# Kernel tuning notes

Hardware: AMD Instinct MI355X
Metric: run time of the kernel (lower is better)

The kernel has to match this reference:

```python
import jax, jax.numpy as jnp
import numpy as np

N_NODES = 50000
N_EDGES = 1600000
N_GRAPHS = 64
IN_DIM = 128
HID = 128
N_CLASSES = 10


def setup_inputs() -> dict:
    key = jax.random.key(0)
    ks = jax.random.split(key, 12)
    x = jax.random.normal(ks[0], (N_NODES, IN_DIM), dtype=jnp.float32)
    edge_index = jax.random.randint(ks[1], (2, N_EDGES), 0, N_NODES, dtype=jnp.int32)
    batch = jnp.sort(jax.random.randint(ks[2], (N_NODES,), 0, N_GRAPHS, dtype=jnp.int32))
    def glorot(k, shape):
        s = 1.0 / np.sqrt(shape[0])
        return jax.random.uniform(k, shape, jnp.float32, -s, s)
    W1 = glorot(ks[3], (IN_DIM, HID)); b1 = jnp.zeros((HID,), jnp.float32)
    W2 = glorot(ks[4], (HID, HID));    b2 = jnp.zeros((HID,), jnp.float32)
    Wc1 = glorot(ks[5], (HID, HID));   bc1 = glorot(ks[6], (HID,))
    Wc2 = glorot(ks[7], (HID, N_CLASSES)); bc2 = glorot(ks[8], (N_CLASSES,))
    return {"x": x, "edge_index": edge_index, "batch": batch,
            "W1": W1, "b1": b1, "W2": W2, "b2": b2,
            "Wc1": Wc1, "bc1": bc1, "Wc2": Wc2, "bc2": bc2}


def gcn_conv(x, edge_index, W, b):
    """PyG GCNConv: sym-normalized A-hat (with self loops) @ (x W) + b."""
    n = x.shape[0]
    loop = jnp.arange(n, dtype=edge_index.dtype)
    src = jnp.concatenate([edge_index[0], loop])  # message source
    dst = jnp.concatenate([edge_index[1], loop])  # message target
    deg = jax.ops.segment_sum(jnp.ones_like(src, dtype=x.dtype), dst, num_segments=n)
    dinv = jnp.where(deg > 0, jax.lax.rsqrt(deg), jnp.zeros_like(deg))
    norm = dinv[src] * dinv[dst]  # [E+N]
    h = x @ W                     # [N, H]
    msg = h[src] * norm[:, None]  # gather + scale
    out = jax.ops.segment_sum(msg, dst, num_segments=n)
    return out + b


def reference(x, edge_index, batch, W1, b1, W2, b2, Wc1, bc1, Wc2, bc2):
    h = jax.nn.relu(gcn_conv(x, edge_index, W1, b1))
    h = jax.nn.relu(gcn_conv(h, edge_index, W2, b2))
    # per-graph mean pooling (segment mean)
    sums = jax.ops.segment_sum(h, batch, num_segments=N_GRAPHS)
    cnt = jax.ops.segment_sum(jnp.ones((h.shape[0],), h.dtype), batch, num_segments=N_GRAPHS)
    g = sums / jnp.clip(cnt, 1.0)[:, None]  # [G, H]
    z = jax.nn.relu(g @ Wc1 + bc1)
    return z @ Wc2 + bc2
```

## Files before the change

kernel.cpp:

```cpp
#include <hip/hip_runtime.h>
#include <cstdint>
#include <cstddef>

#define CHUNK 8192

typedef __attribute__((ext_vector_type(8))) short short8;
typedef __attribute__((ext_vector_type(4))) float f32x4;
typedef __attribute__((ext_vector_type(2))) float f32x2;
typedef __attribute__((ext_vector_type(4))) unsigned int u32x4;

__device__ __forceinline__ float bf2f(unsigned short u) {
  return __uint_as_float(((unsigned)u) << 16);
}
__device__ __forceinline__ unsigned short f2bf(float f) {
  unsigned u = __float_as_uint(f);
  u += 0x7fffu + ((u >> 16) & 1u);
  return (unsigned short)(u >> 16);
}
__device__ __forceinline__ f32x2 unpk(unsigned u) {
  f32x2 r;
  r.x = __uint_as_float(u << 16);
  r.y = __uint_as_float(u & 0xffff0000u);
  return r;
}
__device__ __forceinline__ void pkfma(f32x2& a, f32x2 b, f32x2 c) {
  asm("v_pk_fma_f32 %0, %1, %2, %0" : "+v"(a) : "v"(b), "v"(c));
}

union SMemX {
  unsigned short ws[128 * 136];
  struct { unsigned sorted[CHUNK];
           int h[256]; int lps[256]; int base_s[256]; int cur[256]; } sc;
  struct { int c[256]; int cur[256]; int sb[256];
           unsigned short colL[12288]; } cf;
};

__global__ void prep_k(const float* __restrict__ W1, const float* __restrict__ W2,
                       unsigned short* __restrict__ W1t, unsigned short* __restrict__ W2t,
                       int* __restrict__ gcur, int B,
                       float* __restrict__ gsums, int GN) {
  int idx = blockIdx.x * 256 + threadIdx.x;
  const float* W = (idx < 16384) ? W1 : W2;
  unsigned short* Wt = (idx < 16384) ? W1t : W2t;
  int i = idx & 16383;
  int k = i >> 7, n = i & 127;
  Wt[n * 128 + k] = f2bf(W[i]);
  if (blockIdx.x == 0 && threadIdx.x < B) gcur[threadIdx.x] = 0;
  if (idx < GN) gsums[idx] = 0.f;
}

template <bool AF32, bool WF32>
__device__ __forceinline__ void gemm_tile(SMemX& sm, const void* Ap,
                                          const void* Wp,
                                          unsigned short* C, int N, int tile) {
  if (WF32) {
    const float* Wf = (const float*)Wp;
    for (int idx = threadIdx.x; idx < 16384; idx += 512) {
      int k = idx >> 7, n = idx & 127;
      sm.ws[n * 136 + k] = f2bf(Wf[idx]);
    }
  } else {
    const unsigned short* Wt = (const unsigned short*)Wp;
    for (int idx = threadIdx.x; idx < 2048; idx += 512) {
      int n = idx >> 4, c = idx & 15;
      *(uint4*)&sm.ws[n * 136 + c * 8] = ((const uint4*)Wt)[idx];
    }
  }
  __syncthreads();
  const int w = threadIdx.x >> 6;
  const int lane = threadIdx.x & 63;
  const int quad = lane >> 4, l16 = lane & 15;
  const int r = tile * 128 + w * 16 + l16;
  f32x4 acc[8] = {};
  #pragma unroll
  for (int ks = 0; ks < 4; ks++) {
    short8 a = {};
    if (r < N) {
      if (AF32) {
        const float* ar = (const float*)Ap + (size_t)r * 128 + ks * 32 + quad * 8;
        float4 u0 = *(const float4*)ar;
        float4 u1 = *(const float4*)(ar + 4);
        a[0] = (short)f2bf(u0.x); a[1] = (short)f2bf(u0.y);
        a[2] = (short)f2bf(u0.z); a[3] = (short)f2bf(u0.w);
        a[4] = (short)f2bf(u1.x); a[5] = (short)f2bf(u1.y);
        a[6] = (short)f2bf(u1.z); a[7] = (short)f2bf(u1.w);
      } else {
        a = *(const short8*)((const unsigned short*)Ap + (size_t)r * 128 + ks * 32 + quad * 8);
      }
    }
    #pragma unroll
    for (int t = 0; t < 8; t++) {
      short8 bF = *(const short8*)&sm.ws[(t * 16 + l16) * 136 + ks * 32 + quad * 8];
      acc[t] = __builtin_amdgcn_mfma_f32_16x16x32_bf16(a, bF, acc[t], 0, 0, 0);
    }
  }
  __syncthreads();
  unsigned short* Cs = sm.ws;
  {
    int rloc = w * 16 + quad * 4;
    #pragma unroll
    for (int t = 0; t < 8; t++)
      #pragma unroll
      for (int rg = 0; rg < 4; rg++)
        Cs[(rloc + rg) * 132 + t * 16 + l16] = f2bf(acc[t][rg]);
  }
  __syncthreads();
  const int r0 = tile * 128;
  for (int idx = threadIdx.x; idx < 2048; idx += 512) {
    int row = idx >> 4, c = idx & 15;
    int rr = r0 + row;
    if (rr < N) {
      uint2 a = *(uint2*)&Cs[row * 132 + c * 8];
      uint2 b = *(uint2*)&Cs[row * 132 + c * 8 + 4];
      ((uint4*)C)[(size_t)rr * 16 + c] = make_uint4(a.x, a.y, b.x, b.y);
    }
  }
}

__global__ __launch_bounds__(512) void scat_gemm1a_k(const int* __restrict__ src,
                                                     const int* __restrict__ dst, int E,
                                                     int* __restrict__ gcur,
                                                     unsigned int* __restrict__ tmp,
                                                     int cap, int B,
                                                     const float* __restrict__ x,
                                                     const float* __restrict__ W1,
                                                     unsigned short* __restrict__ B2, int N,
                                                     int nblk, int T1,
                                                     const float* __restrict__ W2,
                                                     unsigned short* __restrict__ W2t,
                                                     int P2) {
  __shared__ SMemX sm;
  const int t = threadIdx.x;
  const int bid = blockIdx.x;
  if (bid >= nblk) {
    int gb = bid - nblk;
    if (gb < T1) {
      gemm_tile<true, true>(sm, x, W1, B2, N, gb);
    } else {
      int base = (gb - T1) * 512 + t;
      for (int i = base; i < 16384; i += P2 * 512) {
        int k = i >> 7, n = i & 127;
        W2t[n * 128 + k] = f2bf(W2[i]);
      }
    }
    return;
  }
  if (t < 256) sm.sc.h[t] = 0;
  __syncthreads();
  int e0 = bid * CHUNK;
  int e1 = e0 + CHUNK; if (e1 > E) e1 = E;
  int m = e1 - e0;
  for (int i = t; i < m; i += 512) {
    atomicAdd(&sm.sc.h[dst[e0 + i] >> 8], 1);
  }
  __syncthreads();
  int v = (t < 256) ? sm.sc.h[t] : 0;
  if (t < 256) sm.sc.lps[t] = v;
  __syncthreads();
  for (int off = 1; off < 256; off <<= 1) {
    int u = (t >= off && t < 256) ? sm.sc.lps[t - off] : 0;
    __syncthreads();
    if (t < 256) sm.sc.lps[t] += u;
    __syncthreads();
  }
  int incl = (t < 256) ? sm.sc.lps[t] : 0;
  if (t < B && v > 0) sm.sc.base_s[t] = atomicAdd(&gcur[t], v);
  if (t < 256) {
    sm.sc.cur[t] = 0;
    sm.sc.lps[t] = incl - v;
  }
  __syncthreads();
  for (int i = t; i < m; i += 512) {
    int d = dst[e0 + i], s = src[e0 + i];
    int b = d >> 8;
    int r = atomicAdd(&sm.sc.cur[b], 1);
    sm.sc.sorted[sm.sc.lps[b] + r] = ((unsigned)b << 24) | ((unsigned)s << 8) | (unsigned)(d & 255);
  }
  __syncthreads();
  for (int i = t; i < m; i += 512) {
    unsigned u = sm.sc.sorted[i];
    int b = u >> 24;
    int p = sm.sc.base_s[b] + (i - sm.sc.lps[b]);
    if (p < cap) tmp[(size_t)b * cap + p] = u;
  }
}

__global__ __launch_bounds__(512) void cnt_gemm1b_k(const unsigned int* __restrict__ tmp,
                                                    const int* __restrict__ gcur,
                                                    int N, int E, int cap, int B,
                                                    float* __restrict__ dinv,
                                                    int* __restrict__ rs,
                                                    unsigned short* __restrict__ col,
                                                    const float* __restrict__ x,
                                                    const float* __restrict__ W1,
                                                    unsigned short* __restrict__ B2,
                                                    int T1) {
  __shared__ SMemX sm;
  const int t = threadIdx.x;
  if ((int)blockIdx.x >= B) {
    gemm_tile<true, true>(sm, x, W1, B2, N, T1 + (int)blockIdx.x - B);
    return;
  }
  int b = blockIdx.x;
  int cb = 0;
  if (t < B) { cb = gcur[t]; if (cb > cap) cb = cap; }
  if (t < 256) sm.cf.sb[t] = cb;
  __syncthreads();
  for (int off = 1; off < 256; off <<= 1) {
    int u = (t >= off && t < 256) ? sm.cf.sb[t - off] : 0;
    __syncthreads();
    if (t < 256) sm.cf.sb[t] += u;
    __syncthreads();
  }
  int base_b = (b > 0) ? sm.cf.sb[b - 1] : 0;
  int cnt_b = sm.cf.sb[b] - base_b;
  if (b == 0 && t == 0) rs[N] = sm.cf.sb[B - 1];
  const unsigned* tb = tmp + (size_t)b * cap;
  if (t < 256) sm.cf.c[t] = 0;
  __syncthreads();
  for (int i = t; i < cnt_b; i += 512) atomicAdd(&sm.cf.c[tb[i] & 255u], 1);
  __syncthreads();
  int v = (t < 256) ? sm.cf.c[t] : 0;
  if (t < 256) sm.cf.cur[t] = v;
  __syncthreads();
  for (int off = 1; off < 256; off <<= 1) {
    int u = (t >= off && t < 256) ? sm.cf.cur[t - off] : 0;
    __syncthreads();
    if (t < 256) sm.cf.cur[t] += u;
    __syncthreads();
  }
  int rsv = (t < 256) ? (base_b + sm.cf.cur[t] - v) : 0;
  int node = (b << 8) + t;
  if (t < 256 && node < N) {
    rs[node] = rsv;
    dinv[node] = rsqrtf((float)v + 1.0f);
  }
  __syncthreads();
  if (cnt_b <= 12288) {
    if (t < 256) sm.cf.cur[t] = rsv - base_b;
    __syncthreads();
    for (int i = t; i < cnt_b; i += 512) {
      unsigned u = tb[i];
      int lpos = atomicAdd(&sm.cf.cur[u & 255u], 1);
      sm.cf.colL[lpos] = (unsigned short)((u >> 8) & 0xFFFFu);
    }
    __syncthreads();
    for (int i = t; i < cnt_b; i += 512) col[base_b + i] = sm.cf.colL[i];
  } else {
    if (t < 256) sm.cf.cur[t] = rsv;
    __syncthreads();
    for (int i = t; i < cnt_b; i += 512) {
      unsigned u = tb[i];
      int pos = atomicAdd(&sm.cf.cur[u & 255u], 1);
      col[pos] = (unsigned short)((u >> 8) & 0xFFFFu);
    }
  }
}

template <bool AF32, bool WF32>
__global__ __launch_bounds__(512) void gemm_bf_k(const void* __restrict__ Ap,
                                                 const void* __restrict__ Wp,
                                                 unsigned short* __restrict__ C, int N) {
  __shared__ SMemX sm;
  gemm_tile<AF32, WF32>(sm, Ap, Wp, C, N, blockIdx.x);
}

template <typename CT>
__device__ __forceinline__ void agg_body(f32x2 (&acc2)[4],
                                         const unsigned short* __restrict__ h,
                                         const CT* __restrict__ col,
                                         const float* __restrict__ dinv,
                                         int beg, int end, int g, int l) {
  int base = beg;
  for (; base + 32 <= end; base += 32) {
    int s[8];
    float w[8];
    uint4 H[8];
    #pragma unroll
    for (int k = 0; k < 8; k++) s[k] = (int)col[base + 4 * k + g];
    #pragma unroll
    for (int k = 0; k < 8; k++) w[k] = dinv[s[k]];
    #pragma unroll
    for (int k = 0; k < 8; k++) H[k] = ((const uint4*)(h + (size_t)s[k] * 128))[l];
    #pragma unroll
    for (int k = 0; k < 8; k++) {
      f32x2 wv; wv.x = w[k]; wv.y = w[k];
      pkfma(acc2[0], unpk(H[k].x), wv);
      pkfma(acc2[1], unpk(H[k].y), wv);
      pkfma(acc2[2], unpk(H[k].z), wv);
      pkfma(acc2[3], unpk(H[k].w), wv);
    }
  }
  for (; base < end; base += 16) {
    int e0 = base + g, e1 = base + 4 + g, e2 = base + 8 + g, e3 = base + 12 + g;
    int i0 = (e0 < end) ? e0 : end - 1;
    int i1 = (e1 < end) ? e1 : end - 1;
    int i2 = (e2 < end) ? e2 : end - 1;
    int i3 = (e3 < end) ? e3 : end - 1;
    int s0 = (int)col[i0], s1 = (int)col[i1], s2 = (int)col[i2], s3 = (int)col[i3];
    float w0 = (e0 < end) ? dinv[s0] : 0.f;
    float w1 = (e1 < end) ? dinv[s1] : 0.f;
    float w2 = (e2 < end) ? dinv[s2] : 0.f;
    float w3 = (e3 < end) ? dinv[s3] : 0.f;
    uint4 h0 = ((const uint4*)(h + (size_t)s0 * 128))[l];
    uint4 h1 = ((const uint4*)(h + (size_t)s1 * 128))[l];
    uint4 h2 = ((const uint4*)(h + (size_t)s2 * 128))[l];
    uint4 h3 = ((const uint4*)(h + (size_t)s3 * 128))[l];
    f32x2 w0v; w0v.x = w0; w0v.y = w0;
    f32x2 w1v; w1v.x = w1; w1v.y = w1;
    f32x2 w2v; w2v.x = w2; w2v.y = w2;
    f32x2 w3v; w3v.x = w3; w3v.y = w3;
    pkfma(acc2[0], unpk(h0.x), w0v); pkfma(acc2[0], unpk(h1.x), w1v);
    pkfma(acc2[0], unpk(h2.x), w2v); pkfma(acc2[0], unpk(h3.x), w3v);
    pkfma(acc2[1], unpk(h0.y), w0v); pkfma(acc2[1], unpk(h1.y), w1v);
    pkfma(acc2[1], unpk(h2.y), w2v); pkfma(acc2[1], unpk(h3.y), w3v);
    pkfma(acc2[2], unpk(h0.z), w0v); pkfma(acc2[2], unpk(h1.z), w1v);
    pkfma(acc2[2], unpk(h2.z), w2v); pkfma(acc2[2], unpk(h3.z), w3v);
    pkfma(acc2[3], unpk(h0.w), w0v); pkfma(acc2[3], unpk(h1.w), w1v);
    pkfma(acc2[3], unpk(h2.w), w2v); pkfma(acc2[3], unpk(h3.w), w3v);
  }
  #pragma unroll
  for (int j = 0; j < 4; j++) {
    acc2[j].x += __shfl_xor(acc2[j].x, 16);
    acc2[j].y += __shfl_xor(acc2[j].y, 16);
    acc2[j].x += __shfl_xor(acc2[j].x, 32);
    acc2[j].y += __shfl_xor(acc2[j].y, 32);
  }
}

template <typename CT>
__global__ __launch_bounds__(256) void agg32_k(const unsigned short* __restrict__ h,
                                               const int* __restrict__ rs,
                                               const CT* __restrict__ col,
                                               const float* __restrict__ dinv,
                                               const float* __restrict__ bias,
                                               unsigned short* __restrict__ outp, int n) {
  int wid = (blockIdx.x * blockDim.x + threadIdx.x) >> 6;
  int lane = threadIdx.x & 63;
  if (wid >= n) return;
  const int g = lane >> 4;
  const int l = lane & 15;
  float di = dinv[wid];
  f32x2 acc2[4];
  {
    uint4 sv = ((const uint4*)(h + (size_t)wid * 128))[l];
    float ws = (g == 0) ? di : 0.f;
    f32x2 wv; wv.x = ws; wv.y = ws;
    acc2[0] = unpk(sv.x) * wv;
    acc2[1] = unpk(sv.y) * wv;
    acc2[2] = unpk(sv.z) * wv;
    acc2[3] = unpk(sv.w) * wv;
  }
  agg_body<CT>(acc2, h, col, dinv, rs[wid], rs[wid + 1], g, l);
  if (g == 0) {
    float4 bA = *(const float4*)(bias + l * 8);
    float4 bB = *(const float4*)(bias + l * 8 + 4);
    float r0 = fmaxf(acc2[0].x * di + bA.x, 0.f);
    float r1 = fmaxf(acc2[0].y * di + bA.y, 0.f);
    float r2 = fmaxf(acc2[1].x * di + bA.z, 0.f);
    float r3 = fmaxf(acc2[1].y * di + bA.w, 0.f);
    float r4 = fmaxf(acc2[2].x * di + bB.x, 0.f);
    float r5 = fmaxf(acc2[2].y * di + bB.y, 0.f);
    float r6 = fmaxf(acc2[3].x * di + bB.z, 0.f);
    float r7 = fmaxf(acc2[3].y * di + bB.w, 0.f);
    u32x4 v;
    v.x = (unsigned)f2bf(r0) | ((unsigned)f2bf(r1) << 16);
    v.y = (unsigned)f2bf(r2) | ((unsigned)f2bf(r3) << 16);
    v.z = (unsigned)f2bf(r4) | ((unsigned)f2bf(r5) << 16);
    v.w = (unsigned)f2bf(r6) | ((unsigned)f2bf(r7) << 16);
    __builtin_nontemporal_store(v, (u32x4*)outp + (size_t)wid * 16 + l);
  }
}

#define SPLITS 8
__global__ __launch_bounds__(256) void pool_sum_k(const unsigned short* __restrict__ h,
                                                  const int* __restrict__ bat, int n,
                                                  float* __restrict__ gsums) {
  __shared__ float red[16][136];
  const int g = blockIdx.x / SPLITS;
  const int sp = blockIdx.x % SPLITS;
  const int t = threadIdx.x;
  const int slot = t >> 4;
  const int seg = t & 15;
  int lo;
  {
    int l = 0, r = n;
    while (l < r) { int m = (l + r) >> 1; if (bat[m] < g) l = m + 1; else r = m; }
    lo = l;
  }
  int hi;
  {
    int l = lo, r = n;
    while (l < r) { int m = (l + r) >> 1; if (bat[m] < g + 1) l = m + 1; else r = m; }
    hi = l;
  }
  int L = hi - lo;
  int chunk = (L + SPLITS - 1) / SPLITS;
  int i0 = lo + sp * chunk;
  int i1 = i0 + chunk; if (i1 > hi) i1 = hi;
  if (i0 >= i1) return;
  float a0 = 0.f, a1 = 0.f, a2 = 0.f, a3 = 0.f, a4 = 0.f, a5 = 0.f, a6 = 0.f, a7 = 0.f;
  for (int i = i0 + slot; i < i1; i += 16) {
    uint4 v = ((const uint4*)(h + (size_t)i * 128))[seg];
    a0 += bf2f((unsigned short)v.x);  a1 += bf2f((unsigned short)(v.x >> 16));
    a2 += bf2f((unsigned short)v.y);  a3 += bf2f((unsigned short)(v.y >> 16));
    a4 += bf2f((unsigned short)v.z);  a5 += bf2f((unsigned short)(v.z >> 16));
    a6 += bf2f((unsigned short)v.w);  a7 += bf2f((unsigned short)(v.w >> 16));
  }
  red[slot][seg * 8 + 0] = a0; red[slot][seg * 8 + 1] = a1;
  red[slot][seg * 8 + 2] = a2; red[slot][seg * 8 + 3] = a3;
  red[slot][seg * 8 + 4] = a4; red[slot][seg * 8 + 5] = a5;
  red[slot][seg * 8 + 6] = a6; red[slot][seg * 8 + 7] = a7;
  __syncthreads();
  if (t < 128) {
    float s = 0.f;
    #pragma unroll
    for (int k = 0; k < 16; k++) s += red[k][t];
    unsafeAtomicAdd(&gsums[g * 128 + t], s);
  }
}

__global__ __launch_bounds__(256) void classify_k(const float* __restrict__ gsums,
                                                  const int* __restrict__ bat, int n,
                                                  const float* __restrict__ Wc1,
                                                  const float* __restrict__ bc1,
                                                  const float* __restrict__ Wc2,
                                                  const float* __restrict__ bc2,
                                                  float* __restrict__ out, int nc) {
  __shared__ float gs[128];
  __shared__ float zs[128];
  const int g = blockIdx.x;
  const int t = threadIdx.x;
  int lo;
  {
    int l = 0, r = n;
    while (l < r) { int m = (l + r) >> 1; if (bat[m] < g) l = m + 1; else r = m; }
    lo = l;
  }
  int hi;
  {
    int l = lo, r = n;
    while (l < r) { int m = (l + r) >> 1; if (bat[m] < g + 1) l = m + 1; else r = m; }
    hi = l;
  }
  if (t < 128) {
    float c = (float)(hi - lo); if (c < 1.f) c = 1.f;
    gs[t] = gsums[g * 128 + t] / c;
  }
  __syncthreads();
  if (t < 128) {
    float a = bc1[t];
    for (int k = 0; k < 128; k++) a += gs[k] * Wc1[k * 128 + t];
    zs[t] = fmaxf(a, 0.f);
  }
  __syncthreads();
  if (t < nc) {
    float o = bc2[t];
    for (int k = 0; k < 128; k++) o += zs[k] * Wc2[k * nc + t];
    out[g * nc + t] = o;
  }
}

__global__ __launch_bounds__(256) void poolclassify2_k(const unsigned short* __restrict__ h,
                                                       const int* __restrict__ bat, int n,
                                                       const float* __restrict__ Wc1,
                                                       const float* __restrict__ bc1,
                                                       const float* __restrict__ Wc2,
                                                       const float* __restrict__ bc2,
                                                       float* __restrict__ out, int nc) {
  __shared__ float red[16][136];
  __shared__ float gs[128];
  __shared__ float zs[128];
  const int g = blockIdx.x;
  const int t = threadIdx.x;
  const int slot = t >> 4;
  const int seg = t & 15;
  int lo;
  {
    int l = 0, r = n;
    while (l < r) { int m = (l + r) >> 1; if (bat[m] < g) l = m + 1; else r = m; }
    lo = l;
  }
  int hi;
  {
    int l = lo, r = n;
    while (l < r) { int m = (l + r) >> 1; if (bat[m] < g + 1) l = m + 1; else r = m; }
    hi = l;
  }
  float a0 = 0.f, a1 = 0.f, a2 = 0.f, a3 = 0.f, a4 = 0.f, a5 = 0.f, a6 = 0.f, a7 = 0.f;
  for (int i = lo + slot; i < hi; i += 16) {
    uint4 v = ((const uint4*)(h + (size_t)i * 128))[seg];
    a0 += bf2f((unsigned short)v.x);  a1 += bf2f((unsigned short)(v.x >> 16));
    a2 += bf2f((unsigned short)v.y);  a3 += bf2f((unsigned short)(v.y >> 16));
    a4 += bf2f((unsigned short)v.z);  a5 += bf2f((unsigned short)(v.z >> 16));
    a6 += bf2f((unsigned short)v.w);  a7 += bf2f((unsigned short)(v.w >> 16));
  }
  red[slot][seg * 8 + 0] = a0; red[slot][seg * 8 + 1] = a1;
  red[slot][seg * 8 + 2] = a2; red[slot][seg * 8 + 3] = a3;
  red[slot][seg * 8 + 4] = a4; red[slot][seg * 8 + 5] = a5;
  red[slot][seg * 8 + 6] = a6; red[slot][seg * 8 + 7] = a7;
  __syncthreads();
  if (t < 128) {
    float c = (float)(hi - lo); if (c < 1.f) c = 1.f;
    float s = 0.f;
    #pragma unroll
    for (int k = 0; k < 16; k++) s += red[k][t];
    gs[t] = s / c;
  }
  __syncthreads();
  if (t < 128) {
    float a = bc1[t];
    for (int k = 0; k < 128; k++) a += gs[k] * Wc1[k * 128 + t];
    zs[t] = fmaxf(a, 0.f);
  }
  __syncthreads();
  if (t < nc) {
    float o = bc2[t];
    for (int k = 0; k < 128; k++) o += zs[k] * Wc2[k * nc + t];
    out[g * nc + t] = o;
  }
}

__global__ void count_edges_k(const int* __restrict__ dst, int E, int* __restrict__ cnt) {
  int e = blockIdx.x * blockDim.x + threadIdx.x;
  if (e < E) atomicAdd(&cnt[dst[e]], 1);
}
__global__ void dinv_k(const int* __restrict__ cnt, float* __restrict__ dinv, int n) {
  int i = blockIdx.x * blockDim.x + threadIdx.x;
  if (i < n) dinv[i] = rsqrtf((float)cnt[i] + 1.0f);
}
__global__ void fill_csr_k(const int* __restrict__ src, const int* __restrict__ dst, int E,
                           int* __restrict__ cursor, int* __restrict__ col) {
  int e = blockIdx.x * blockDim.x + threadIdx.x;
  if (e < E) {
    int d = dst[e], s = src[e];
    int pos = atomicAdd(&cursor[d], 1);
    col[pos] = s;
  }
}
__global__ void scan1_k(const int* __restrict__ cnt, int* __restrict__ rs,
                        int* __restrict__ partials, int n) {
  __shared__ int s[1024];
  int t = threadIdx.x;
  int gid = blockIdx.x * 1024 + t;
  int v = (gid < n) ? cnt[gid] : 0;
  s[t] = v;
  __syncthreads();
  for (int off = 1; off < 1024; off <<= 1) {
    int u = (t >= off) ? s[t - off] : 0;
    __syncthreads();
    s[t] += u;
    __syncthreads();
  }
  if (gid < n) rs[gid] = s[t] - v;
  if (t == 1023) partials[blockIdx.x] = s[1023];
}
__global__ void scan2_k(int* __restrict__ partials, int nb) {
  if (threadIdx.x == 0 && blockIdx.x == 0) {
    int acc = 0;
    for (int i = 0; i < nb; i++) { int v = partials[i]; partials[i] = acc; acc += v; }
  }
}
__global__ void scan3_k(int* __restrict__ rs, int* __restrict__ cursor,
                        const int* __restrict__ partials, int n, int total) {
  int gid = blockIdx.x * blockDim.x + threadIdx.x;
  if (gid < n) {
    int v = rs[gid] + partials[gid >> 10];
    rs[gid] = v;
    cursor[gid] = v;
  }
  if (gid == 0) rs[n] = total;
}

extern "C" void kernel_launch(void* const* d_in, const int* in_sizes, int n_in,
                              void* d_out, int out_size, void* d_ws, size_t ws_size,
                              hipStream_t stream) {
  const float* x   = (const float*)d_in[0];
  const int*   ei  = (const int*)d_in[1];
  const int*   bat = (const int*)d_in[2];
  const float* W1  = (const float*)d_in[3];
  const float* b1  = (const float*)d_in[4];
  const float* W2  = (const float*)d_in[5];
  const float* b2  = (const float*)d_in[6];
  const float* Wc1 = (const float*)d_in[7];
  const float* bc1 = (const float*)d_in[8];
  const float* Wc2 = (const float*)d_in[9];
  const float* bc2 = (const float*)d_in[10];
  float* out = (float*)d_out;

  const int N  = in_sizes[0] / 128;
  const int E  = in_sizes[1] / 2;
  const int NC = in_sizes[10];
  const int G  = out_size / NC;
  const int* src = ei;
  const int* dst = ei + E;
  (void)n_in; (void)ws_size;

  size_t off = 0;
  auto walloc = [&](size_t bytes) -> void* {
    void* p = (char*)d_ws + off;
    off += (bytes + 255) & ~(size_t)255;
    return p;
  };
  unsigned short* B2 = (unsigned short*)walloc((size_t)N * 128 * 2);
  unsigned short* B3 = (unsigned short*)walloc((size_t)N * 128 * 2);
  unsigned short* W1t = (unsigned short*)walloc(128 * 128 * 2);
  unsigned short* W2t = (unsigned short*)walloc(128 * 128 * 2);
  float* dinv = (float*)walloc((size_t)N * 4);
  int*   rs   = (int*)  walloc((size_t)(N + 1) * 4);
  float* gsums = (float*)walloc((size_t)G * 128 * 4);
  int*   gcur  = (int*)walloc(256 * 4);

  const bool small = (N <= 65535);
  const int gblocks = (N + 127) / 128;
  const int aggGrid = (N + 3) / 4;

  if (small) {
    const int B    = (N + 255) >> 8;
    const int nblk = (E + CHUNK - 1) / CHUNK;
    const int cap  = (E + B - 1) / B + 2048;
    const int T1   = (gblocks * 3) / 5;
    const int P2   = 8;
    unsigned short* col = (unsigned short*)walloc((size_t)E * 2);
    unsigned int*   tmp = (unsigned int*)  walloc((size_t)B * cap * 4);

    (void)hipMemsetAsync(gsums, 0, (size_t)G * 128 * 4 + 1024, stream);
    scat_gemm1a_k<<<nblk + T1 + P2, 512, 0, stream>>>(src, dst, E, gcur, tmp, cap, B,
                                                      x, W1, B2, N, nblk, T1, W2, W2t, P2);
    cnt_gemm1b_k<<<B + (gblocks - T1), 512, 0, stream>>>(tmp, gcur, N, E, cap, B,
                                                         dinv, rs, col, x, W1, B2, T1);
    agg32_k<unsigned short><<<aggGrid, 256, 0, stream>>>(B2, rs, col, dinv, b1, B3, N);
    gemm_bf_k<false, false><<<gblocks, 512, 0, stream>>>(B3, W2t, B2, N);
    agg32_k<unsigned short><<<aggGrid, 256, 0, stream>>>(B2, rs, col, dinv, b2, B3, N);
    pool_sum_k<<<G * SPLITS, 256, 0, stream>>>(B3, bat, N, gsums);
    classify_k<<<G, 256, 0, stream>>>(gsums, bat, N, Wc1, bc1, Wc2, bc2, out, NC);
  } else {
    const int nb = (N + 1023) / 1024;
    int* cnt    = (int*)walloc((size_t)N * 4);
    int* cursor = (int*)walloc((size_t)N * 4);
    int* col    = (int*)walloc((size_t)E * 4);
    int* partials = (int*)walloc(256 * 4);
    prep_k<<<128, 256, 0, stream>>>(W1, W2, W1t, W2t, cnt , 0, gsums, G * 128);
    (void)hipMemsetAsync(cnt, 0, (size_t)N * 4, stream);
    count_edges_k<<<(E + 255) / 256, 256, 0, stream>>>(dst, E, cnt);
    scan1_k<<<nb, 1024, 0, stream>>>(cnt, rs, partials, N);
    scan2_k<<<1, 64, 0, stream>>>(partials, nb);
    scan3_k<<<(N + 255) / 256, 256, 0, stream>>>(rs, cursor, partials, N, E);
    dinv_k<<<(N + 255) / 256, 256, 0, stream>>>(cnt, dinv, N);
    fill_csr_k<<<(E + 255) / 256, 256, 0, stream>>>(src, dst, E, cursor, col);

    gemm_bf_k<true, false><<<gblocks, 512, 0, stream>>>(x, W1t, B2, N);
    agg32_k<int><<<aggGrid, 256, 0, stream>>>(B2, rs, col, dinv, b1, B3, N);
    gemm_bf_k<false, false><<<gblocks, 512, 0, stream>>>(B3, W2t, B2, N);
    agg32_k<int><<<aggGrid, 256, 0, stream>>>(B2, rs, col, dinv, b2, B3, N);
    poolclassify2_k<<<G, 256, 0, stream>>>(B3, bat, N, Wc1, bc1, Wc2, bc2, out, NC);
  }
}
```

Before: 259.2 us.

## Fuse full GCN pipeline into one cooperative persistent kernel with grid syncs

```diff
diff --git a/kernel.cpp b/kernel.cpp
--- a/kernel.cpp
+++ b/kernel.cpp
@@ -1,8 +1,12 @@
 #include <hip/hip_runtime.h>
+#include <hip/hip_cooperative_groups.h>
 #include <cstdint>
 #include <cstddef>
 
+namespace cg = cooperative_groups;
+
 #define CHUNK 8192
+#define SPLITS 8
 
 typedef __attribute__((ext_vector_type(8))) short short8;
 typedef __attribute__((ext_vector_type(4))) float f32x4;
@@ -33,21 +37,9 @@
            int h[256]; int lps[256]; int base_s[256]; int cur[256]; } sc;
   struct { int c[256]; int cur[256]; int sb[256];
            unsigned short colL[12288]; } cf;
+  struct { float red[16][136]; } pl;
+  struct { float gs[128]; float zs[128]; } cl;
 };
-
-__global__ void prep_k(const float* __restrict__ W1, const float* __restrict__ W2,
-                       unsigned short* __restrict__ W1t, unsigned short* __restrict__ W2t,
-                       int* __restrict__ gcur, int B,
-                       float* __restrict__ gsums, int GN) {
-  int idx = blockIdx.x * 256 + threadIdx.x;
-  const float* W = (idx < 16384) ? W1 : W2;
-  unsigned short* Wt = (idx < 16384) ? W1t : W2t;
-  int i = idx & 16383;
-  int k = i >> 7, n = i & 127;
-  Wt[n * 128 + k] = f2bf(W[i]);
-  if (blockIdx.x == 0 && threadIdx.x < B) gcur[threadIdx.x] = 0;
-  if (idx < GN) gsums[idx] = 0.f;
-}
 
 template <bool AF32, bool WF32>
 __device__ __forceinline__ void gemm_tile(SMemX& sm, const void* Ap,
@@ -117,37 +109,15 @@
   }
 }
 
-__global__ __launch_bounds__(512) void scat_gemm1a_k(const int* __restrict__ src,
-                                                     const int* __restrict__ dst, int E,
-                                                     int* __restrict__ gcur,
-                                                     unsigned int* __restrict__ tmp,
-                                                     int cap, int B,
-                                                     const float* __restrict__ x,
-                                                     const float* __restrict__ W1,
-                                                     unsigned short* __restrict__ B2, int N,
-                                                     int nblk, int T1,
-                                                     const float* __restrict__ W2,
-                                                     unsigned short* __restrict__ W2t,
-                                                     int P2) {
-  __shared__ SMemX sm;
+__device__ __forceinline__ void scatter_block(SMemX& sm, const int* __restrict__ src,
+                                              const int* __restrict__ dst, int E,
+                                              int* __restrict__ gcur,
+                                              unsigned int* __restrict__ tmp,
+                                              int cap, int B, int cblk) {
   const int t = threadIdx.x;
-  const int bid = blockIdx.x;
-  if (bid >= nblk) {
-    int gb = bid - nblk;
-    if (gb < T1) {
-      gemm_tile<true, true>(sm, x, W1, B2, N, gb);
-    } else {
-      int base = (gb - T1) * 512 + t;
-      for (int i = base; i < 16384; i += P2 * 512) {
-        int k = i >> 7, n = i & 127;
-        W2t[n * 128 + k] = f2bf(W2[i]);
-      }
-    }
-    return;
-  }
   if (t < 256) sm.sc.h[t] = 0;
   __syncthreads();
-  int e0 = bid * CHUNK;
+  int e0 = cblk * CHUNK;
   int e1 = e0 + CHUNK; if (e1 > E) e1 = E;
   int m = e1 - e0;
   for (int i = t; i < m; i += 512) {
@@ -183,25 +153,16 @@
     int p = sm.sc.base_s[b] + (i - sm.sc.lps[b]);
     if (p < cap) tmp[(size_t)b * cap + p] = u;
   }
-}
-
-__global__ __launch_bounds__(512) void cnt_gemm1b_k(const unsigned int* __restrict__ tmp,
-                                                    const int* __restrict__ gcur,
-                                                    int N, int E, int cap, int B,
-                                                    float* __restrict__ dinv,
-                                                    int* __restrict__ rs,
-                                                    unsigned short* __restrict__ col,
-                                                    const float* __restrict__ x,
-                                                    const float* __restrict__ W1,
-                                                    unsigned short* __restrict__ B2,
-                                                    int T1) {
-  __shared__ SMemX sm;
+  __syncthreads();
+}
+
+__device__ __forceinline__ void cntfill_block(SMemX& sm, const unsigned int* __restrict__ tmp,
+                                              const int* __restrict__ gcur,
+                                              int N, int cap, int B,
+                                              float* __restrict__ dinv,
+                                              int* __restrict__ rs,
+                                              unsigned short* __restrict__ col, int b) {
   const int t = threadIdx.x;
-  if ((int)blockIdx.x >= B) {
-    gemm_tile<true, true>(sm, x, W1, B2, N, T1 + (int)blockIdx.x - B);
-    return;
-  }
-  int b = blockIdx.x;
   int cb = 0;
   if (t < B) { cb = gcur[t]; if (cb > cap) cb = cap; }
   if (t < 256) sm.cf.sb[t] = cb;
@@ -255,14 +216,7 @@
       col[pos] = (unsigned short)((u >> 8) & 0xFFFFu);
     }
   }
-}
-
-template <bool AF32, bool WF32>
-__global__ __launch_bounds__(512) void gemm_bf_k(const void* __restrict__ Ap,
-                                                 const void* __restrict__ Wp,
-                                                 unsigned short* __restrict__ C, int N) {
-  __shared__ SMemX sm;
-  gemm_tile<AF32, WF32>(sm, Ap, Wp, C, N, blockIdx.x);
+  __syncthreads();
 }
 
 template <typename CT>
@@ -329,6 +283,245 @@
 }
 
 template <typename CT>
+__device__ __forceinline__ void agg_phase(const unsigned short* __restrict__ h,
+                                          const int* __restrict__ rs,
+                                          const CT* __restrict__ col,
+                                          const float* __restrict__ dinv,
+                                          const float* __restrict__ bias,
+                                          unsigned short* __restrict__ outp,
+                                          int n, int bid, int NB) {
+  const int t = threadIdx.x;
+  const int w = t >> 6;
+  const int lane = t & 63;
+  const int g = lane >> 4;
+  const int l = lane & 15;
+  for (int wid = bid * 8 + w; wid < n; wid += NB * 8) {
+    float di = dinv[wid];
+    f32x2 acc2[4];
+    {
+      uint4 sv = ((const uint4*)(h + (size_t)wid * 128))[l];
+      float ws = (g == 0) ? di : 0.f;
+      f32x2 wv; wv.x = ws; wv.y = ws;
+      acc2[0] = unpk(sv.x) * wv;
+      acc2[1] = unpk(sv.y) * wv;
+      acc2[2] = unpk(sv.z) * wv;
+      acc2[3] = unpk(sv.w) * wv;
+    }
+    agg_body<CT>(acc2, h, col, dinv, rs[wid], rs[wid + 1], g, l);
+    if (g == 0) {
+      float4 bA = *(const float4*)(bias + l * 8);
+      float4 bB = *(const float4*)(bias + l * 8 + 4);
+      float r0 = fmaxf(acc2[0].x * di + bA.x, 0.f);
+      float r1 = fmaxf(acc2[0].y * di + bA.y, 0.f);
+      float r2 = fmaxf(acc2[1].x * di + bA.z, 0.f);
+      float r3 = fmaxf(acc2[1].y * di + bA.w, 0.f);
+      float r4 = fmaxf(acc2[2].x * di + bB.x, 0.f);
+      float r5 = fmaxf(acc2[2].y * di + bB.y, 0.f);
+      float r6 = fmaxf(acc2[3].x * di + bB.z, 0.f);
+      float r7 = fmaxf(acc2[3].y * di + bB.w, 0.f);
+      u32x4 v;
+      v.x = (unsigned)f2bf(r0) | ((unsigned)f2bf(r1) << 16);
+      v.y = (unsigned)f2bf(r2) | ((unsigned)f2bf(r3) << 16);
+      v.z = (unsigned)f2bf(r4) | ((unsigned)f2bf(r5) << 16);
+      v.w = (unsigned)f2bf(r6) | ((unsigned)f2bf(r7) << 16);
+      __builtin_nontemporal_store(v, (u32x4*)outp + (size_t)wid * 16 + l);
+    }
+  }
+}
+
+__device__ __forceinline__ void pool_block(SMemX& sm, const unsigned short* __restrict__ h,
+                                           const int* __restrict__ bat, int n,
+                                           float* __restrict__ gsums, int s) {
+  const int t = threadIdx.x;
+  const int g = s / SPLITS;
+  const int sp = s % SPLITS;
+  const int slot = (t >> 4) & 15;
+  const int seg = t & 15;
+  int lo;
+  { int l = 0, r = n; while (l < r) { int m = (l + r) >> 1; if (bat[m] < g) l = m + 1; else r = m; } lo = l; }
+  int hi;
+  { int l = lo, r = n; while (l < r) { int m = (l + r) >> 1; if (bat[m] < g + 1) l = m + 1; else r = m; } hi = l; }
+  int L = hi - lo;
+  int chunk = (L + SPLITS - 1) / SPLITS;
+  int i0 = lo + sp * chunk;
+  int i1 = i0 + chunk; if (i1 > hi) i1 = hi;
+  if (i0 >= i1) return;
+  if (t < 256) {
+    float a0 = 0.f, a1 = 0.f, a2 = 0.f, a3 = 0.f, a4 = 0.f, a5 = 0.f, a6 = 0.f, a7 = 0.f;
+    for (int i = i0 + slot; i < i1; i += 16) {
+      uint4 v = ((const uint4*)(h + (size_t)i * 128))[seg];
+      a0 += bf2f((unsigned short)v.x);  a1 += bf2f((unsigned short)(v.x >> 16));
+      a2 += bf2f((unsigned short)v.y);  a3 += bf2f((unsigned short)(v.y >> 16));
+      a4 += bf2f((unsigned short)v.z);  a5 += bf2f((unsigned short)(v.z >> 16));
+      a6 += bf2f((unsigned short)v.w);  a7 += bf2f((unsigned short)(v.w >> 16));
+    }
+    sm.pl.red[slot][seg * 8 + 0] = a0; sm.pl.red[slot][seg * 8 + 1] = a1;
+    sm.pl.red[slot][seg * 8 + 2] = a2; sm.pl.red[slot][seg * 8 + 3] = a3;
+    sm.pl.red[slot][seg * 8 + 4] = a4; sm.pl.red[slot][seg * 8 + 5] = a5;
+    sm.pl.red[slot][seg * 8 + 6] = a6; sm.pl.red[slot][seg * 8 + 7] = a7;
+  }
+  __syncthreads();
+  if (t < 128) {
+    float ssum = 0.f;
+    #pragma unroll
+    for (int k = 0; k < 16; k++) ssum += sm.pl.red[k][t];
+    unsafeAtomicAdd(&gsums[g * 128 + t], ssum);
+  }
+  __syncthreads();
+}
+
+__device__ __forceinline__ void classify_block(SMemX& sm, const float* __restrict__ gsums,
+                                               const int* __restrict__ bat, int n,
+                                               const float* __restrict__ Wc1,
+                                               const float* __restrict__ bc1,
+                                               const float* __restrict__ Wc2,
+                                               const float* __restrict__ bc2,
+                                               float* __restrict__ out, int nc, int g) {
+  const int t = threadIdx.x;
+  int lo;
+  { int l = 0, r = n; while (l < r) { int m = (l + r) >> 1; if (bat[m] < g) l = m + 1; else r = m; } lo = l; }
+  int hi;
+  { int l = lo, r = n; while (l < r) { int m = (l + r) >> 1; if (bat[m] < g + 1) l = m + 1; else r = m; } hi = l; }
+  if (t < 128) {
+    float c = (float)(hi - lo); if (c < 1.f) c = 1.f;
+    sm.cl.gs[t] = gsums[g * 128 + t] / c;
+  }
+  __syncthreads();
+  if (t < 128) {
+    float a = bc1[t];
+    for (int k = 0; k < 128; k++) a += sm.cl.gs[k] * Wc1[k * 128 + t];
+    sm.cl.zs[t] = fmaxf(a, 0.f);
+  }
+  __syncthreads();
+  if (t < nc) {
+    float o = bc2[t];
+    for (int k = 0; k < 128; k++) o += sm.cl.zs[k] * Wc2[k * nc + t];
+    out[g * nc + t] = o;
+  }
+  __syncthreads();
+}
+
+__global__ __launch_bounds__(512) void mega_k(
+    const int* __restrict__ src, const int* __restrict__ dst, int E,
+    int* __restrict__ gcur, unsigned int* __restrict__ tmp, int cap, int B,
+    const float* __restrict__ x, const float* __restrict__ W1,
+    const float* __restrict__ W2,
+    const float* __restrict__ b1v, const float* __restrict__ b2v,
+    const int* __restrict__ bat,
+    const float* __restrict__ Wc1, const float* __restrict__ bc1,
+    const float* __restrict__ Wc2, const float* __restrict__ bc2,
+    float* __restrict__ out, int NC, int G,
+    unsigned short* __restrict__ B2, unsigned short* __restrict__ B3,
+    float* __restrict__ dinv, int* __restrict__ rs,
+    unsigned short* __restrict__ col,
+    float* __restrict__ gsums, int N, int nblk, int gblocks) {
+  __shared__ SMemX sm;
+  cg::grid_group grid = cg::this_grid();
+  const int t = threadIdx.x;
+  const int bid = blockIdx.x;
+  const int NB = gridDim.x;
+  for (int i = bid * 512 + t; i < G * 128; i += NB * 512) gsums[i] = 0.f;
+  if (bid == 0 && t < 256) gcur[t] = 0;
+  grid.sync();
+  for (int c = bid; c < nblk; c += NB) scatter_block(sm, src, dst, E, gcur, tmp, cap, B, c);
+  grid.sync();
+  if (bid < B) {
+    cntfill_block(sm, tmp, gcur, N, cap, B, dinv, rs, col, bid);
+  } else {
+    for (int tile = bid - B; tile < gblocks; tile += NB - B) {
+      gemm_tile<true, true>(sm, x, W1, B2, N, tile);
+      __syncthreads();
+    }
+  }
+  grid.sync();
+  agg_phase<unsigned short>(B2, rs, col, dinv, b1v, B3, N, bid, NB);
+  grid.sync();
+  for (int tile = bid; tile < gblocks; tile += NB) {
+    gemm_tile<false, true>(sm, B3, W2, B2, N, tile);
+    __syncthreads();
+  }
+  grid.sync();
+  agg_phase<unsigned short>(B2, rs, col, dinv, b2v, B3, N, bid, NB);
+  grid.sync();
+  for (int s = bid; s < G * SPLITS; s += NB) pool_block(sm, B3, bat, N, gsums, s);
+  grid.sync();
+  for (int g = bid; g < G; g += NB)
+    classify_block(sm, gsums, bat, N, Wc1, bc1, Wc2, bc2, out, NC, g);
+}
+
+
+__global__ void prep_k(const float* __restrict__ W1, const float* __restrict__ W2,
+                       unsigned short* __restrict__ W1t, unsigned short* __restrict__ W2t,
+                       int* __restrict__ gcur, int B,
+                       float* __restrict__ gsums, int GN) {
+  int idx = blockIdx.x * 256 + threadIdx.x;
+  const float* W = (idx < 16384) ? W1 : W2;
+  unsigned short* Wt = (idx < 16384) ? W1t : W2t;
+  int i = idx & 16383;
+  int k = i >> 7, n = i & 127;
+  Wt[n * 128 + k] = f2bf(W[i]);
+  if (blockIdx.x == 0 && threadIdx.x < B) gcur[threadIdx.x] = 0;
+  if (idx < GN) gsums[idx] = 0.f;
+}
+
+__global__ __launch_bounds__(512) void scat_gemm1a_k(const int* __restrict__ src,
+                                                     const int* __restrict__ dst, int E,
+                                                     int* __restrict__ gcur,
+                                                     unsigned int* __restrict__ tmp,
+                                                     int cap, int B,
+                                                     const float* __restrict__ x,
+                                                     const float* __restrict__ W1,
+                                                     unsigned short* __restrict__ B2, int N,
+                                                     int nblk, int T1,
+                                                     const float* __restrict__ W2,
+                                                     unsigned short* __restrict__ W2t,
+                                                     int P2) {
+  __shared__ SMemX sm;
+  const int t = threadIdx.x;
+  const int bid = blockIdx.x;
+  if (bid >= nblk) {
+    int gb = bid - nblk;
+    if (gb < T1) {
+      gemm_tile<true, true>(sm, x, W1, B2, N, gb);
+    } else {
+      int base = (gb - T1) * 512 + t;
+      for (int i = base; i < 16384; i += P2 * 512) {
+        int k = i >> 7, n = i & 127;
+        W2t[n * 128 + k] = f2bf(W2[i]);
+      }
+    }
+    return;
+  }
+  scatter_block(sm, src, dst, E, gcur, tmp, cap, B, bid);
+}
+
+__global__ __launch_bounds__(512) void cnt_gemm1b_k(const unsigned int* __restrict__ tmp,
+                                                    const int* __restrict__ gcur,
+                                                    int N, int E, int cap, int B,
+                                                    float* __restrict__ dinv,
+                                                    int* __restrict__ rs,
+                                                    unsigned short* __restrict__ col,
+                                                    const float* __restrict__ x,
+                                                    const float* __restrict__ W1,
+                                                    unsigned short* __restrict__ B2,
+                                                    int T1) {
+  __shared__ SMemX sm;
+  if ((int)blockIdx.x >= B) {
+    gemm_tile<true, true>(sm, x, W1, B2, N, T1 + (int)blockIdx.x - B);
+    return;
+  }
+  cntfill_block(sm, tmp, gcur, N, cap, B, dinv, rs, col, blockIdx.x);
+}
+
+template <bool AF32, bool WF32>
+__global__ __launch_bounds__(512) void gemm_bf_k(const void* __restrict__ Ap,
+                                                 const void* __restrict__ Wp,
+                                                 unsigned short* __restrict__ C, int N) {
+  __shared__ SMemX sm;
+  gemm_tile<AF32, WF32>(sm, Ap, Wp, C, N, blockIdx.x);
+}
+
+template <typename CT>
 __global__ __launch_bounds__(256) void agg32_k(const unsigned short* __restrict__ h,
                                                const int* __restrict__ rs,
                                                const CT* __restrict__ col,
@@ -372,7 +565,6 @@
   }
 }
 
-#define SPLITS 8
 __global__ __launch_bounds__(256) void pool_sum_k(const unsigned short* __restrict__ h,
                                                   const int* __restrict__ bat, int n,
                                                   float* __restrict__ gsums) {
@@ -383,17 +575,9 @@
   const int slot = t >> 4;
   const int seg = t & 15;
   int lo;
-  {
-    int l = 0, r = n;
-    while (l < r) { int m = (l + r) >> 1; if (bat[m] < g) l = m + 1; else r = m; }
-    lo = l;
-  }
+  { int l = 0, r = n; while (l < r) { int m = (l + r) >> 1; if (bat[m] < g) l = m + 1; else r = m; } lo = l; }
   int hi;
-  {
-    int l = lo, r = n;
-    while (l < r) { int m = (l + r) >> 1; if (bat[m] < g + 1) l = m + 1; else r = m; }
-    hi = l;
-  }
+  { int l = lo, r = n; while (l < r) { int m = (l + r) >> 1; if (bat[m] < g + 1) l = m + 1; else r = m; } hi = l; }
   int L = hi - lo;
   int chunk = (L + SPLITS - 1) / SPLITS;
   int i0 = lo + sp * chunk;
@@ -432,17 +616,9 @@
   const int g = blockIdx.x;
   const int t = threadIdx.x;
   int lo;
-  {
-    int l = 0, r = n;
-    while (l < r) { int m = (l + r) >> 1; if (bat[m] < g) l = m + 1; else r = m; }
-    lo = l;
-  }
+  { int l = 0, r = n; while (l < r) { int m = (l + r) >> 1; if (bat[m] < g) l = m + 1; else r = m; } lo = l; }
   int hi;
-  {
-    int l = lo, r = n;
-    while (l < r) { int m = (l + r) >> 1; if (bat[m] < g + 1) l = m + 1; else r = m; }
-    hi = l;
-  }
+  { int l = lo, r = n; while (l < r) { int m = (l + r) >> 1; if (bat[m] < g + 1) l = m + 1; else r = m; } hi = l; }
   if (t < 128) {
     float c = (float)(hi - lo); if (c < 1.f) c = 1.f;
     gs[t] = gsums[g * 128 + t] / c;
@@ -476,17 +652,9 @@
   const int slot = t >> 4;
   const int seg = t & 15;
   int lo;
-  {
-    int l = 0, r = n;
-    while (l < r) { int m = (l + r) >> 1; if (bat[m] < g) l = m + 1; else r = m; }
-    lo = l;
-  }
+  { int l = 0, r = n; while (l < r) { int m = (l + r) >> 1; if (bat[m] < g) l = m + 1; else r = m; } lo = l; }
   int hi;
-  {
-    int l = lo, r = n;
-    while (l < r) { int m = (l + r) >> 1; if (bat[m] < g + 1) l = m + 1; else r = m; }
-    hi = l;
-  }
+  { int l = lo, r = n; while (l < r) { int m = (l + r) >> 1; if (bat[m] < g + 1) l = m + 1; else r = m; } hi = l; }
   float a0 = 0.f, a1 = 0.f, a2 = 0.f, a3 = 0.f, a4 = 0.f, a5 = 0.f, a6 = 0.f, a7 = 0.f;
   for (int i = lo + slot; i < hi; i += 16) {
     uint4 v = ((const uint4*)(h + (size_t)i * 128))[seg];
@@ -570,6 +738,50 @@
     cursor[gid] = v;
   }
   if (gid == 0) rs[n] = total;
+}
+
+template <typename CT>
+__global__ __launch_bounds__(256) void agg32i_k(const unsigned short* __restrict__ h,
+                                                const int* __restrict__ rs,
+                                                const CT* __restrict__ col,
+                                                const float* __restrict__ dinv,
+                                                const float* __restrict__ bias,
+                                                unsigned short* __restrict__ outp, int n) {
+  int wid = (blockIdx.x * blockDim.x + threadIdx.x) >> 6;
+  int lane = threadIdx.x & 63;
+  if (wid >= n) return;
+  const int g = lane >> 4;
+  const int l = lane & 15;
+  float di = dinv[wid];
+  f32x2 acc2[4];
+  {
+    uint4 sv = ((const uint4*)(h + (size_t)wid * 128))[l];
+    float ws = (g == 0) ? di : 0.f;
+    f32x2 wv; wv.x = ws; wv.y = ws;
+    acc2[0] = unpk(sv.x) * wv;
+    acc2[1] = unpk(sv.y) * wv;
+    acc2[2] = unpk(sv.z) * wv;
+    acc2[3] = unpk(sv.w) * wv;
+  }
+  agg_body<CT>(acc2, h, col, dinv, rs[wid], rs[wid + 1], g, l);
+  if (g == 0) {
+    float4 bA = *(const float4*)(bias + l * 8);
+    float4 bB = *(const float4*)(bias + l * 8 + 4);
+    float r0 = fmaxf(acc2[0].x * di + bA.x, 0.f);
+    float r1 = fmaxf(acc2[0].y * di + bA.y, 0.f);
+    float r2 = fmaxf(acc2[1].x * di + bA.z, 0.f);
+    float r3 = fmaxf(acc2[1].y * di + bA.w, 0.f);
+    float r4 = fmaxf(acc2[2].x * di + bB.x, 0.f);
+    float r5 = fmaxf(acc2[2].y * di + bB.y, 0.f);
+    float r6 = fmaxf(acc2[3].x * di + bB.z, 0.f);
+    float r7 = fmaxf(acc2[3].y * di + bB.w, 0.f);
+    u32x4 v;
+    v.x = (unsigned)f2bf(r0) | ((unsigned)f2bf(r1) << 16);
+    v.y = (unsigned)f2bf(r2) | ((unsigned)f2bf(r3) << 16);
+    v.z = (unsigned)f2bf(r4) | ((unsigned)f2bf(r5) << 16);
+    v.w = (unsigned)f2bf(r6) | ((unsigned)f2bf(r7) << 16);
+    __builtin_nontemporal_store(v, (u32x4*)outp + (size_t)wid * 16 + l);
+  }
 }
 
 extern "C" void kernel_launch(void* const* d_in, const int* in_sizes, int n_in,
@@ -619,26 +831,70 @@
     const int B    = (N + 255) >> 8;
     const int nblk = (E + CHUNK - 1) / CHUNK;
     const int cap  = (E + B - 1) / B + 2048;
-    const int T1   = (gblocks * 3) / 5;
-    const int P2   = 8;
     unsigned short* col = (unsigned short*)walloc((size_t)E * 2);
     unsigned int*   tmp = (unsigned int*)  walloc((size_t)B * cap * 4);
 
-    (void)hipMemsetAsync(gsums, 0, (size_t)G * 128 * 4 + 1024, stream);
-    scat_gemm1a_k<<<nblk + T1 + P2, 512, 0, stream>>>(src, dst, E, gcur, tmp, cap, B,
-                                                      x, W1, B2, N, nblk, T1, W2, W2t, P2);
-    cnt_gemm1b_k<<<B + (gblocks - T1), 512, 0, stream>>>(tmp, gcur, N, E, cap, B,
-                                                         dinv, rs, col, x, W1, B2, T1);
-    agg32_k<unsigned short><<<aggGrid, 256, 0, stream>>>(B2, rs, col, dinv, b1, B3, N);
-    gemm_bf_k<false, false><<<gblocks, 512, 0, stream>>>(B3, W2t, B2, N);
-    agg32_k<unsigned short><<<aggGrid, 256, 0, stream>>>(B2, rs, col, dinv, b2, B3, N);
-    pool_sum_k<<<G * SPLITS, 256, 0, stream>>>(B3, bat, N, gsums);
-    classify_k<<<G, 256, 0, stream>>>(gsums, bat, N, Wc1, bc1, Wc2, bc2, out, NC);
+    static int s_coopBlocks = -2;
+    if (s_coopBlocks == -2) {
+      s_coopBlocks = -1;
+      int dev = 0;
+      if (hipGetDevice(&dev) == hipSuccess) {
+        hipDeviceProp_t prop;
+        if (hipGetDeviceProperties(&prop, dev) == hipSuccess) {
+          int perCU = 0;
+          if (hipOccupancyMaxActiveBlocksPerMultiprocessor(&perCU, (const void*)mega_k, 512, 0) == hipSuccess && perCU > 0)
+            s_coopBlocks = perCU * prop.multiProcessorCount;
+        }
+      }
+    }
+
+    bool usedCoop = false;
+    if (s_coopBlocks > B + 8) {
+      const int* a_src = src; const int* a_dst = dst; int a_E = E;
+      int* a_gcur = gcur; unsigned int* a_tmp = tmp; int a_cap = cap; int a_B = B;
+      const float* a_x = x; const float* a_W1 = W1; const float* a_W2 = W2;
+      const float* a_b1 = b1; const float* a_b2 = b2; const int* a_bat = bat;
+      const float* a_Wc1 = Wc1; const float* a_bc1 = bc1;
+      const float* a_Wc2 = Wc2; const float* a_bc2 = bc2;
+      float* a_out = out; int a_NC = NC; int a_G = G;
+      unsigned short* a_B2 = B2; unsigned short* a_B3 = B3;
+      float* a_dinv = dinv; int* a_rs = rs; unsigned short* a_col = col;
+      float* a_gsums = gsums; int a_N = N; int a_nblk = nblk; int a_gblocks = gblocks;
+      void* kargs[] = {
+        (void*)&a_src, (void*)&a_dst, (void*)&a_E,
+        (void*)&a_gcur, (void*)&a_tmp, (void*)&a_cap, (void*)&a_B,
+        (void*)&a_x, (void*)&a_W1, (void*)&a_W2,
+        (void*)&a_b1, (void*)&a_b2, (void*)&a_bat,
+        (void*)&a_Wc1, (void*)&a_bc1, (void*)&a_Wc2, (void*)&a_bc2,
+        (void*)&a_out, (void*)&a_NC, (void*)&a_G,
+        (void*)&a_B2, (void*)&a_B3,
+        (void*)&a_dinv, (void*)&a_rs, (void*)&a_col,
+        (void*)&a_gsums, (void*)&a_N, (void*)&a_nblk, (void*)&a_gblocks };
+      if (hipLaunchCooperativeKernel((const void*)mega_k, dim3(s_coopBlocks), dim3(512),
+                                     kargs, 0, stream) == hipSuccess) {
+        usedCoop = true;
+      }
+    }
+
+    if (!usedCoop) {
+      const int T1 = (gblocks * 3) / 5;
+      const int P2 = 8;
+      (void)hipMemsetAsync(gsums, 0, (size_t)G * 128 * 4 + 1024, stream);
+      scat_gemm1a_k<<<nblk + T1 + P2, 512, 0, stream>>>(src, dst, E, gcur, tmp, cap, B,
+                                                        x, W1, B2, N, nblk, T1, W2, W2t, P2);
+      cnt_gemm1b_k<<<B + (gblocks - T1), 512, 0, stream>>>(tmp, gcur, N, E, cap, B,
+                                                           dinv, rs, col, x, W1, B2, T1);
+      agg32_k<unsigned short><<<aggGrid, 256, 0, stream>>>(B2, rs, col, dinv, b1, B3, N);
+      gemm_bf_k<false, false><<<gblocks, 512, 0, stream>>>(B3, W2t, B2, N);
+      agg32_k<unsigned short><<<aggGrid, 256, 0, stream>>>(B2, rs, col, dinv, b2, B3, N);
+      pool_sum_k<<<G * SPLITS, 256, 0, stream>>>(B3, bat, N, gsums);
+      classify_k<<<G, 256, 0, stream>>>(gsums, bat, N, Wc1, bc1, Wc2, bc2, out, NC);
+    }
   } else {
     const int nb = (N + 1023) / 1024;
     int* cnt    = (int*)walloc((size_t)N * 4);
     int* cursor = (int*)walloc((size_t)N * 4);
-    int* col    = (int*)walloc((size_t)E * 4);
+    int* coli   = (int*)walloc((size_t)E * 4);
     int* partials = (int*)walloc(256 * 4);
     prep_k<<<128, 256, 0, stream>>>(W1, W2, W1t, W2t, cnt , 0, gsums, G * 128);
     (void)hipMemsetAsync(cnt, 0, (size_t)N * 4, stream);
@@ -647,12 +903,12 @@
     scan2_k<<<1, 64, 0, stream>>>(partials, nb);
     scan3_k<<<(N + 255) / 256, 256, 0, stream>>>(rs, cursor, partials, N, E);
     dinv_k<<<(N + 255) / 256, 256, 0, stream>>>(cnt, dinv, N);
-    fill_csr_k<<<(E + 255) / 256, 256, 0, stream>>>(src, dst, E, cursor, col);
+    fill_csr_k<<<(E + 255) / 256, 256, 0, stream>>>(src, dst, E, cursor, coli);
 
     gemm_bf_k<true, false><<<gblocks, 512, 0, stream>>>(x, W1t, B2, N);
-    agg32_k<int><<<aggGrid, 256, 0, stream>>>(B2, rs, col, dinv, b1, B3, N);
+    agg32i_k<int><<<aggGrid, 256, 0, stream>>>(B2, rs, coli, dinv, b1, B3, N);
     gemm_bf_k<false, false><<<gblocks, 512, 0, stream>>>(B3, W2t, B2, N);
-    agg32_k<int><<<aggGrid, 256, 0, stream>>>(B2, rs, col, dinv, b2, B3, N);
+    agg32i_k<int><<<aggGrid, 256, 0, stream>>>(B2, rs, coli, dinv, b2, B3, N);
     poolclassify2_k<<<G, 256, 0, stream>>>(B3, bat, N, Wc1, bc1, Wc2, bc2, out, NC);
   }
 }
```

Result: slower. 577.4 us (+122.7%).
